# Kernel tuning notes

Hardware: AMD Instinct MI355X
Metric: run time of the kernel (lower is better)

The kernel has to match this reference:

```python
import jax, jax.numpy as jnp
import numpy as np

N, D, H, O, E = 50000, 512, 512, 256, 150000
NEG_SLOPE = 0.2
EPS = 1e-16


def gat_conv(x, edge_index, W_src, W_dst, a_src, a_dst, bias):
    """Single-head PyG GATConv, add_self_loops=False.
    x: [N, Din]; edge_index: [2, E] (row 0 = src, row 1 = dst).
    W_src/W_dst: [Din, C]; a_src/a_dst: [C]; bias: [C].
    """
    src, dst = edge_index[0], edge_index[1]
    h_src = x @ W_src                      # [N, C]
    h_dst = x @ W_dst                      # [N, C]
    alpha_src = h_src @ a_src              # [N]
    alpha_dst = h_dst @ a_dst              # [N]
    e = jax.nn.leaky_relu(alpha_src[src] + alpha_dst[dst], NEG_SLOPE)  # [E]
    # per-destination segment softmax (numerically stable)
    m = jax.ops.segment_max(e, dst, num_segments=N)       # [N]
    ex = jnp.exp(e - m[dst])                               # [E]
    s = jax.ops.segment_sum(ex, dst, num_segments=N)       # [N]
    alpha = ex / (s[dst] + EPS)                            # [E]
    # scatter-add weighted source messages to destinations
    out = jax.ops.segment_sum(alpha[:, None] * h_src[src], dst, num_segments=N)  # [N, C]
    return out + bias


def setup_inputs() -> dict:
    key = jax.random.key(0)
    ks = jax.random.split(key, 20)
    g = lambda i, shape, sc: (jax.random.normal(ks[i], shape, dtype=jnp.float32) * sc)
    inp = {
        "x": jax.random.normal(ks[0], (N, D), dtype=jnp.float32),
        "edge_index": jax.random.randint(ks[1], (2, E), 0, N, dtype=jnp.int32),
        "edge_index_2_hop": jax.random.randint(ks[2], (2, E), 0, N, dtype=jnp.int32),
        # conv1 (D -> H)
        "W1_src": g(3, (D, H), 0.05), "W1_dst": g(4, (D, H), 0.05),
        "a1_src": g(5, (H,), 0.05), "a1_dst": g(6, (H,), 0.05),
        "b1": jnp.zeros((H,), jnp.float32),
        # lin1 (H -> H)
        "Wl1": g(7, (H, H), 0.05), "bl1": jnp.zeros((H,), jnp.float32),
        # conv2 (H -> O)
        "W2_src": g(8, (H, O), 0.05), "W2_dst": g(9, (H, O), 0.05),
        "a2_src": g(10, (O,), 0.05), "a2_dst": g(11, (O,), 0.05),
        "b2": jnp.zeros((O,), jnp.float32),
        # lin2 (O -> O)
        "Wl2": g(12, (O, O), 0.05), "bl2": jnp.zeros((O,), jnp.float32),
    }
    return inp


def reference(x, edge_index, edge_index_2_hop,
              W1_src, W1_dst, a1_src, a1_dst, b1, Wl1, bl1,
              W2_src, W2_dst, a2_src, a2_dst, b2, Wl2, bl2):
    h = (gat_conv(x, edge_index, W1_src, W1_dst, a1_src, a1_dst, b1)
         + gat_conv(x, edge_index_2_hop, W1_src, W1_dst, a1_src, a1_dst, b1))
    h = jax.nn.relu(h @ Wl1 + bl1)
    h = (gat_conv(h, edge_index, W2_src, W2_dst, a2_src, a2_dst, b2)
         + gat_conv(h, edge_index_2_hop, W2_src, W2_dst, a2_src, a2_dst, b2))
    return h @ Wl2 + bl2
```

## Files before the change

### kernel.cpp

```cpp
#include <hip/hip_runtime.h>

typedef unsigned short u16;
typedef __attribute__((ext_vector_type(8))) unsigned short v8u16;
typedef __attribute__((ext_vector_type(4))) unsigned short v4u16;
typedef __attribute__((ext_vector_type(8))) __bf16 v8bf;
typedef __attribute__((ext_vector_type(4))) float v4f;

#define NN 50000
#define EE 150000
#define SCAN_CHUNK 512
#define NB_PER_SET 98

__device__ inline float b2f(u16 u) {
    union { unsigned int i; float f; } x; x.i = ((unsigned int)u) << 16; return x.f;
}
__device__ inline u16 f2b(float f) {
    union { float f; unsigned int i; } x; x.f = f;
    unsigned int r = x.i + 0x7FFFu + ((x.i >> 16) & 1u);
    return (u16)(r >> 16);
}
__device__ inline float wred(float v) {
    v += __shfl_down(v, 32, 64);
    v += __shfl_down(v, 16, 64);
    v += __shfl_down(v, 8, 64);
    v += __shfl_down(v, 4, 64);
    v += __shfl_down(v, 2, 64);
    v += __shfl_down(v, 1, 64);
    return v;
}
__device__ inline int wred_i(int v) {
    v += __shfl_down(v, 32, 64);
    v += __shfl_down(v, 16, 64);
    v += __shfl_down(v, 8, 64);
    v += __shfl_down(v, 4, 64);
    v += __shfl_down(v, 2, 64);
    v += __shfl_down(v, 1, 64);
    return v;
}

__device__ __forceinline__ void gll16(const u16* g, u16* l) {
    __builtin_amdgcn_global_load_lds(
        (const __attribute__((address_space(1))) void*)g,
        (__attribute__((address_space(3))) void*)l, 16, 0, 0);
}


__global__ void transpose4t(const float* __restrict__ W0, u16* __restrict__ T0,
                            const float* __restrict__ W1, u16* __restrict__ T1,
                            const float* __restrict__ W2, u16* __restrict__ T2,
                            const float* __restrict__ W3, u16* __restrict__ T3) {
    int b = blockIdx.x;
    const float* W; u16* T; int N, K, t;
    if (b < 256)      { W = W0; T = T0; K = 512; N = 512; t = b; }
    else if (b < 512) { W = W1; T = T1; K = 512; N = 512; t = b - 256; }
    else if (b < 640) { W = W2; T = T2; K = 512; N = 256; t = b - 512; }
    else              { W = W3; T = T3; K = 256; N = 256; t = b - 640; }
    const int tilesN = N >> 5;
    const int kb = (t / tilesN) << 5;
    const int nb = (t % tilesN) << 5;
    __shared__ u16 tile[32][33];
    const int c = threadIdx.x & 31;
    const int r0 = threadIdx.x >> 5;
#pragma unroll
    for (int rr = 0; rr < 4; ++rr) {
        int r = r0 + rr * 8;
        tile[r][c] = f2b(W[(size_t)(kb + r) * N + nb + c]);
    }
    __syncthreads();
#pragma unroll
    for (int rr = 0; rr < 4; ++rr) {
        int r = r0 + rr * 8;
        T[(size_t)(nb + r) * K + kb + c] = tile[c][r];
    }
}

__global__ void wv4(const float* __restrict__ Wa, const float* __restrict__ Wb,
                    const float* __restrict__ Wc, const float* __restrict__ Wd,
                    const float* __restrict__ aa, const float* __restrict__ ab,
                    const float* __restrict__ ac, const float* __restrict__ ad,
                    float* __restrict__ vbuf) {
    int rw = (blockIdx.x * blockDim.x + threadIdx.x) >> 6;
    int lane = threadIdx.x & 63;
    if (rw >= 2048) return;
    int seg = rw >> 9, r = rw & 511;
    const float* W; const float* a; int C;
    if (seg == 0)      { W = Wa; a = aa; C = 512; }
    else if (seg == 1) { W = Wb; a = ab; C = 512; }
    else if (seg == 2) { W = Wc; a = ac; C = 256; }
    else               { W = Wd; a = ad; C = 256; }
    float s = 0.f;
    int c0 = lane * 8;
    if (c0 < C) {
        const float* wp = W + (size_t)r * C + c0;
        v4f w0 = *(const v4f*)wp;
        v4f w1 = *(const v4f*)(wp + 4);
        v4f a0 = *(const v4f*)(a + c0);
        v4f a1 = *(const v4f*)(a + c0 + 4);
#pragma unroll
        for (int j = 0; j < 4; ++j) s += w0[j] * a0[j] + w1[j] * a1[j];
    }
    s = wred(s);
    if (lane == 0) vbuf[rw] = s;
}

__global__ void alpha_pair_f32x(const float* __restrict__ X, const float* __restrict__ vs,
                                const float* __restrict__ vd, float* __restrict__ as_,
                                float* __restrict__ ad_, u16* __restrict__ Xb, int Nn) {
    int w = (blockIdx.x * blockDim.x + threadIdx.x) >> 6;
    int lane = threadIdx.x & 63;
    if (w >= Nn) return;
    const float* xp = X + (size_t)w * 512 + lane * 8;
    v4f x0 = *(const v4f*)xp;
    v4f x1 = *(const v4f*)(xp + 4);
    const float* vsp = vs + lane * 8;
    const float* vdp = vd + lane * 8;
    float s1 = 0.f, s2 = 0.f;
    v8u16 o;
#pragma unroll
    for (int j = 0; j < 4; ++j) {
        s1 += x0[j] * vsp[j] + x1[j] * vsp[j + 4];
        s2 += x0[j] * vdp[j] + x1[j] * vdp[j + 4];
        o[j] = f2b(x0[j]); o[j + 4] = f2b(x1[j]);
    }
    *(v8u16*)(Xb + (size_t)w * 512 + lane * 8) = o;
    s1 = wred(s1);
    s2 = wred(s2);
    if (lane == 0) { as_[w] = s1; ad_[w] = s2; }
}


__global__ void deg2_kernel(const int* __restrict__ ei1, const int* __restrict__ ei2,
                            int* __restrict__ deg) {
    int idx = blockIdx.x * blockDim.x + threadIdx.x;
    if (idx >= 2 * EE) return;
    int set = idx >= EE;
    int e = idx - set * EE;
    const int* ei = set ? ei2 : ei1;
    atomicAdd(&deg[set * NN + ei[EE + e]], 1);
}

__global__ void scan_partial(const int* __restrict__ deg, int* __restrict__ bsum) {
    int b = blockIdx.x;
    int set = b / NB_PER_SET, lb = b - set * NB_PER_SET;
    int tid = threadIdx.x;
    int i0 = lb * SCAN_CHUNK + tid * 2;
    int s = 0;
    if (i0 < NN)     s += deg[set * NN + i0];
    if (i0 + 1 < NN) s += deg[set * NN + i0 + 1];
    s = wred_i(s);
    __shared__ int lsum[4];
    if ((tid & 63) == 0) lsum[tid >> 6] = s;
    __syncthreads();
    if (tid == 0) bsum[b] = lsum[0] + lsum[1] + lsum[2] + lsum[3];
}

__global__ void scan_tops(int* __restrict__ bsum) {
    __shared__ int ls[256];
    int tid = threadIdx.x;
    int set = tid >> 7, lb = tid & 127;
    int v = (lb < NB_PER_SET) ? bsum[set * NB_PER_SET + lb] : 0;
    ls[tid] = v;
    __syncthreads();
    for (int off = 1; off < 128; off <<= 1) {
        int t = (lb >= off) ? ls[tid - off] : 0;
        __syncthreads();
        ls[tid] += t;
        __syncthreads();
    }
    if (lb < NB_PER_SET) bsum[set * NB_PER_SET + lb] = ls[tid] - v;
}

__global__ void scan_final(const int* __restrict__ deg, const int* __restrict__ bsum,
                           int* __restrict__ rp) {
    int b = blockIdx.x;
    int set = b / NB_PER_SET, lb = b - set * NB_PER_SET;
    int tid = threadIdx.x;
    int i0 = lb * SCAN_CHUNK + tid * 2;
    int d0 = (i0 < NN)     ? deg[set * NN + i0]     : 0;
    int d1 = (i0 + 1 < NN) ? deg[set * NN + i0 + 1] : 0;
    int pair = d0 + d1;
    __shared__ int ps[256];
    ps[tid] = pair;
    __syncthreads();
    for (int off = 1; off < 256; off <<= 1) {
        int t = (tid >= off) ? ps[tid - off] : 0;
        __syncthreads();
        ps[tid] += t;
        __syncthreads();
    }
    int base = bsum[b] + ps[tid] - pair;
    if (i0 < NN)     rp[set * (NN + 1) + i0] = base;
    if (i0 + 1 < NN) rp[set * (NN + 1) + i0 + 1] = base + d0;
    if (b == 0 && tid == 0) { rp[NN] = EE; rp[(NN + 1) + NN] = EE; }
}

__global__ void fill2_kernel(const int* __restrict__ ei1, const int* __restrict__ ei2,
                             const int* __restrict__ rp, int* __restrict__ deg,
                             int* __restrict__ srcp) {
    int idx = blockIdx.x * blockDim.x + threadIdx.x;
    if (idx >= 2 * EE) return;
    int set = idx >= EE;
    int e = idx - set * EE;
    const int* ei = set ? ei2 : ei1;
    int d = ei[EE + e];
    int old = atomicSub(&deg[set * NN + d], 1);
    int pos = rp[set * (NN + 1) + d] + old - 1;
    srcp[set * EE + pos] = ei[e];
}

template <int CV>
__global__ void gat_pull(const int* __restrict__ rp, const int* __restrict__ srcp,
                         const float* __restrict__ asrc, const float* __restrict__ adst,
                         const u16* __restrict__ H, const float* __restrict__ bias,
                         u16* __restrict__ G, int Nn) {
    const int C = CV * 64;
    int d = (blockIdx.x * blockDim.x + threadIdx.x) >> 6;
    int lane = threadIdx.x & 63;
    if (d >= Nn) return;
    const float ad = adst[d];
    float out[CV];
#pragma unroll
    for (int j = 0; j < CV; ++j) out[j] = 0.f;
#pragma unroll
    for (int set = 0; set < 2; ++set) {
        const int* rpS = rp + set * (NN + 1);
        const int* srcS = srcp + set * EE;
        int beg = rpS[d], end = rpS[d + 1];
        float acc[CV];
#pragma unroll
        for (int j = 0; j < CV; ++j) acc[j] = 0.f;
        float ssum = 0.f;
        int n = end - beg;
        if (n > 0) {
            if constexpr (CV == 8) {
                int s0 = srcS[beg];
                float a0 = asrc[s0];
                v8u16 h0 = *(const v8u16*)(H + (size_t)s0 * C + lane * 8);
                float a1 = 0.f; v8u16 h1{};
                if (n > 1) {
                    int s1 = srcS[beg + 1];
                    a1 = asrc[s1];
                    h1 = *(const v8u16*)(H + (size_t)s1 * C + lane * 8);
                }
                for (int i = beg + 2; i < end; ++i) {
                    int s2 = srcS[i];
                    float a2 = asrc[s2];
                    v8u16 h2 = *(const v8u16*)(H + (size_t)s2 * C + lane * 8);
                    float t = a0 + ad; t = t > 0.f ? t : 0.2f * t;
                    float w = __expf(fminf(t, 60.f));
                    ssum += w;
#pragma unroll
                    for (int j = 0; j < 8; ++j) acc[j] += w * b2f(h0[j]);
                    a0 = a1; h0 = h1; a1 = a2; h1 = h2;
                }
                if (n > 1) {
                    float t = a0 + ad; t = t > 0.f ? t : 0.2f * t;
                    float w = __expf(fminf(t, 60.f));
                    ssum += w;
#pragma unroll
                    for (int j = 0; j < 8; ++j) acc[j] += w * b2f(h0[j]);
                    a0 = a1; h0 = h1;
                }
                float t = a0 + ad; t = t > 0.f ? t : 0.2f * t;
                float w = __expf(fminf(t, 60.f));
                ssum += w;
#pragma unroll
                for (int j = 0; j < 8; ++j) acc[j] += w * b2f(h0[j]);
            } else {
                int s0 = srcS[beg];
                float a0 = asrc[s0];
                v4u16 h0 = *(const v4u16*)(H + (size_t)s0 * C + lane * 4);
                float a1 = 0.f; v4u16 h1{};
                if (n > 1) {
                    int s1 = srcS[beg + 1];
                    a1 = asrc[s1];
                    h1 = *(const v4u16*)(H + (size_t)s1 * C + lane * 4);
                }
                for (int i = beg + 2; i < end; ++i) {
                    int s2 = srcS[i];
                    float a2 = asrc[s2];
                    v4u16 h2 = *(const v4u16*)(H + (size_t)s2 * C + lane * 4);
                    float t = a0 + ad; t = t > 0.f ? t : 0.2f * t;
                    float w = __expf(fminf(t, 60.f));
                    ssum += w;
#pragma unroll
                    for (int j = 0; j < 4; ++j) acc[j] += w * b2f(h0[j]);
                    a0 = a1; h0 = h1; a1 = a2; h1 = h2;
                }
                if (n > 1) {
                    float t = a0 + ad; t = t > 0.f ? t : 0.2f * t;
                    float w = __expf(fminf(t, 60.f));
                    ssum += w;
#pragma unroll
                    for (int j = 0; j < 4; ++j) acc[j] += w * b2f(h0[j]);
                    a0 = a1; h0 = h1;
                }
                float t = a0 + ad; t = t > 0.f ? t : 0.2f * t;
                float w = __expf(fminf(t, 60.f));
                ssum += w;
#pragma unroll
                for (int j = 0; j < 4; ++j) acc[j] += w * b2f(h0[j]);
            }
        }
        float inv = 1.f / (ssum + 1e-16f);
#pragma unroll
        for (int j = 0; j < CV; ++j) out[j] += acc[j] * inv;
    }
    const float* bp = bias + lane * CV;
    u16* gp = G + (size_t)d * C + lane * CV;
    if constexpr (CV == 8) {
        v8u16 o;
#pragma unroll
        for (int j = 0; j < 8; ++j) o[j] = f2b(out[j] + 2.f * bp[j]);
        *(v8u16*)gp = o;
    } else {
        v4u16 o;
#pragma unroll
        for (int j = 0; j < 4; ++j) o[j] = f2b(out[j] + 2.f * bp[j]);
        *(v4u16*)gp = o;
    }
}

__global__ __launch_bounds__(256, 3) void gemm_bf16(
    const u16* __restrict__ A, const u16* __restrict__ Bt, void* __restrict__ Cv,
    int M, int N, int K, const float* __restrict__ bias, int relu, int outf32,
    const float* __restrict__ avs, const float* __restrict__ avd,
    float* __restrict__ aout_s, float* __restrict__ aout_d) {
    __shared__ u16 As[128 * 32];
    __shared__ u16 Bs[128 * 32];
    const int tid = threadIdx.x;
    const int lane = tid & 63;
    const int wid = tid >> 6;
    const int wm = wid >> 1;
    const int wn = wid & 1;
    const int quad = lane >> 4;
    const int l16 = lane & 15;
    const int tileM = blockIdx.y * 128;
    const int tileN = blockIdx.x * 128;

    const int srow = tid >> 2;
    const int scol = (tid & 3) * 8;
    int ra0 = tileM + srow;       if (ra0 >= M) ra0 = M - 1;
    int ra1 = tileM + 64 + srow;  if (ra1 >= M) ra1 = M - 1;
    const u16* gA0 = A + (size_t)ra0 * K + scol;
    const u16* gA1 = A + (size_t)ra1 * K + scol;
    const u16* gB0 = Bt + (size_t)(tileN + srow) * K + scol;
    const u16* gB1 = Bt + (size_t)(tileN + 64 + srow) * K + scol;
    u16* lA0 = As + wid * 512;
    u16* lA1 = As + 2048 + wid * 512;
    u16* lB0 = Bs + wid * 512;
    u16* lB1 = Bs + 2048 + wid * 512;

    v4f acc[4][4];
#pragma unroll
    for (int i = 0; i < 4; ++i)
#pragma unroll
        for (int j = 0; j < 4; ++j) acc[i][j] = v4f{0.f, 0.f, 0.f, 0.f};

    for (int k0 = 0; k0 < K; k0 += 32) {
        gll16(gA0 + k0, lA0);
        gll16(gA1 + k0, lA1);
        gll16(gB0 + k0, lB0);
        gll16(gB1 + k0, lB1);
        __syncthreads();
        v8bf af[4], bfr[4];
#pragma unroll
        for (int i = 0; i < 4; ++i)
            af[i] = __builtin_bit_cast(v8bf, *(const v8u16*)&As[(wm * 64 + i * 16 + l16) * 32 + quad * 8]);
#pragma unroll
        for (int i = 0; i < 4; ++i)
            bfr[i] = __builtin_bit_cast(v8bf, *(const v8u16*)&Bs[(wn * 64 + i * 16 + l16) * 32 + quad * 8]);
#pragma unroll
        for (int mi = 0; mi < 4; ++mi)
#pragma unroll
            for (int ni = 0; ni < 4; ++ni)
                acc[mi][ni] = __builtin_amdgcn_mfma_f32_16x16x32_bf16(af[mi], bfr[ni], acc[mi][ni], 0, 0, 0);
        __syncthreads();
    }

    float rs[4][4], rd[4][4];
#pragma unroll
    for (int mi = 0; mi < 4; ++mi)
#pragma unroll
        for (int rr = 0; rr < 4; ++rr) { rs[mi][rr] = 0.f; rd[mi][rr] = 0.f; }

#pragma unroll
    for (int mi = 0; mi < 4; ++mi)
#pragma unroll
        for (int ni = 0; ni < 4; ++ni) {
            int col = tileN + wn * 64 + ni * 16 + l16;
            float bb = bias ? bias[col] : 0.f;
            float ws_ = avs ? avs[col] : 0.f;
            float wd_ = avd ? avd[col] : 0.f;
            int row0 = tileM + wm * 64 + mi * 16 + quad * 4;
#pragma unroll
            for (int rr = 0; rr < 4; ++rr) {
                int row = row0 + rr;
                if (row < M) {
                    float v = acc[mi][ni][rr] + bb;
                    if (relu) v = fmaxf(v, 0.f);
                    if (outf32) ((float*)Cv)[(size_t)row * N + col] = v;
                    else        ((u16*)Cv)[(size_t)row * N + col] = f2b(v);
                    rs[mi][rr] += v * ws_;
                    rd[mi][rr] += v * wd_;
                }
            }
        }

    if (avs) {
#pragma unroll
        for (int mi = 0; mi < 4; ++mi)
#pragma unroll
            for (int rr = 0; rr < 4; ++rr) {
                int row = tileM + wm * 64 + mi * 16 + quad * 4 + rr;
                float a = rs[mi][rr], b = rd[mi][rr];
                a += __shfl_down(a, 8, 64); a += __shfl_down(a, 4, 64);
                a += __shfl_down(a, 2, 64); a += __shfl_down(a, 1, 64);
                b += __shfl_down(b, 8, 64); b += __shfl_down(b, 4, 64);
                b += __shfl_down(b, 2, 64); b += __shfl_down(b, 1, 64);
                if (l16 == 0 && row < M) {
                    atomicAdd(&aout_s[row], a);
                    atomicAdd(&aout_d[row], b);
                }
            }
    }
}


extern "C" void kernel_launch(void* const* d_in, const int* in_sizes, int n_in,
                              void* d_out, int out_size, void* d_ws, size_t ws_size,
                              hipStream_t stream) {
    const float* x  = (const float*)d_in[0];
    const int* ei1  = (const int*)d_in[1];
    const int* ei2  = (const int*)d_in[2];
    const float* W1s = (const float*)d_in[3];
    const float* W1d = (const float*)d_in[4];
    const float* a1s = (const float*)d_in[5];
    const float* a1d = (const float*)d_in[6];
    const float* b1  = (const float*)d_in[7];
    const float* Wl1 = (const float*)d_in[8];
    const float* bl1 = (const float*)d_in[9];
    const float* W2s = (const float*)d_in[10];
    const float* W2d = (const float*)d_in[11];
    const float* a2s = (const float*)d_in[12];
    const float* a2d = (const float*)d_in[13];
    const float* b2  = (const float*)d_in[14];
    const float* Wl2 = (const float*)d_in[15];
    const float* bl2 = (const float*)d_in[16];
    float* out = (float*)d_out;

    char* ws = (char*)d_ws;
    size_t off = 0;
    auto alloc = [&](size_t b) { void* p = ws + off; off = (off + b + 255) & ~(size_t)255; return p; };
    u16* bufA   = (u16*)alloc((size_t)NN * 512 * 2);
    u16* bufB   = (u16*)alloc((size_t)NN * 512 * 2);
    int* rp     = (int*)alloc((size_t)2 * (NN + 1) * 4);
    int* srcp   = (int*)alloc((size_t)2 * EE * 4);
    int* zblk   = (int*)alloc((size_t)4 * NN * 4);
    int* deg    = zblk;
    float* asrc2 = (float*)(zblk + 2 * NN);
    float* adst2 = (float*)(zblk + 3 * NN);
    int* bsum   = (int*)alloc((size_t)2 * NB_PER_SET * 4);
    float* asrc = (float*)alloc((size_t)NN * 4);
    float* adst = (float*)alloc((size_t)NN * 4);
    float* vbuf = (float*)alloc(2048 * 4);
    u16* Wt1s   = (u16*)alloc((size_t)512 * 512 * 2);
    u16* Wtl1   = (u16*)alloc((size_t)512 * 512 * 2);
    u16* Wt2s   = (u16*)alloc((size_t)512 * 256 * 2);
    u16* Wtl2   = (u16*)alloc((size_t)256 * 256 * 2);
    u16* g2buf  = bufB + (size_t)NN * 256;

    hipMemsetAsync(zblk, 0, (size_t)4 * NN * 4, stream);
    deg2_kernel<<<(2 * EE + 255) / 256, 256, 0, stream>>>(ei1, ei2, deg);
    scan_partial<<<2 * NB_PER_SET, 256, 0, stream>>>(deg, bsum);
    scan_tops<<<1, 256, 0, stream>>>(bsum);
    scan_final<<<2 * NB_PER_SET, 256, 0, stream>>>(deg, bsum, rp);
    fill2_kernel<<<(2 * EE + 255) / 256, 256, 0, stream>>>(ei1, ei2, rp, deg, srcp);

    transpose4t<<<704, 256, 0, stream>>>(W1s, Wt1s, Wl1, Wtl1, W2s, Wt2s, Wl2, Wtl2);
    wv4<<<512, 256, 0, stream>>>(W1s, W1d, W2s, W2d, a1s, a1d, a2s, a2d, vbuf);

    alpha_pair_f32x<<<(NN + 3) / 4, 256, 0, stream>>>(x, vbuf, vbuf + 512, asrc, adst, bufB, NN);
    gemm_bf16<<<dim3(4, 391), 256, 0, stream>>>(bufB, Wt1s, bufA, NN, 512, 512, nullptr, 0, 0,
                                                nullptr, nullptr, nullptr, nullptr);
    gat_pull<8><<<(NN + 3) / 4, 256, 0, stream>>>(rp, srcp, asrc, adst, bufA, b1, bufB, NN);
    gemm_bf16<<<dim3(4, 391), 256, 0, stream>>>(bufB, Wtl1, bufA, NN, 512, 512, bl1, 1, 0,
                                                vbuf + 1024, vbuf + 1536, asrc2, adst2);

    gemm_bf16<<<dim3(2, 391), 256, 0, stream>>>(bufA, Wt2s, bufB, NN, 256, 512, nullptr, 0, 0,
                                                nullptr, nullptr, nullptr, nullptr);
    gat_pull<4><<<(NN + 3) / 4, 256, 0, stream>>>(rp, srcp, asrc2, adst2, bufB, b2, g2buf, NN);
    gemm_bf16<<<dim3(2, 391), 256, 0, stream>>>(g2buf, Wtl2, out, NN, 256, 256, bl2, 0, 1,
                                                nullptr, nullptr, nullptr, nullptr);

    (void)in_sizes; (void)n_in; (void)out_size; (void)ws_size;
}
```

Baseline: 514.6 us.

## Rewrite bf16 GEMM with 256x256 tiles, 4-stage LDS pipeline and swizzle

Replaces the 128x128 single-buffered GEMM with a 512-thread, 256x256-tile kernel. It uses a 4-deep ring of LDS buffers loaded asynchronously with explicit vmcnt waits, an XOR swizzle on LDS columns to reduce bank conflicts, and raised wave priority around the MFMA block. The aim is to overlap global loads with MFMA work and raise data reuse per tile. In exchange it uses much more LDS and more registers, and gives fewer blocks for the N=256 GEMMs, which risks lower occupancy and load imbalance.

```diff
diff --git a/kernel.cpp b/kernel.cpp
--- a/kernel.cpp
+++ b/kernel.cpp
@@ -321,78 +321,104 @@
     }
 }
 
-__global__ __launch_bounds__(256, 3) void gemm_bf16(
+__global__ __launch_bounds__(512, 2) void gemm_dp(
     const u16* __restrict__ A, const u16* __restrict__ Bt, void* __restrict__ Cv,
     int M, int N, int K, const float* __restrict__ bias, int relu, int outf32,
     const float* __restrict__ avs, const float* __restrict__ avd,
     float* __restrict__ aout_s, float* __restrict__ aout_d) {
-    __shared__ u16 As[128 * 32];
-    __shared__ u16 Bs[128 * 32];
+    __shared__ u16 As[4 * 8192];
+    __shared__ u16 Bs[4 * 8192];
     const int tid = threadIdx.x;
     const int lane = tid & 63;
     const int wid = tid >> 6;
-    const int wm = wid >> 1;
-    const int wn = wid & 1;
+    const int wm = wid >> 2;
+    const int wn = wid & 3;
     const int quad = lane >> 4;
     const int l16 = lane & 15;
-    const int tileM = blockIdx.y * 128;
-    const int tileN = blockIdx.x * 128;
+    const int tileM = blockIdx.y * 256;
+    const int tileN = blockIdx.x * 256;
 
     const int srow = tid >> 2;
-    const int scol = (tid & 3) * 8;
-    int ra0 = tileM + srow;       if (ra0 >= M) ra0 = M - 1;
-    int ra1 = tileM + 64 + srow;  if (ra1 >= M) ra1 = M - 1;
+    const int scol = 8 * ((tid & 3) ^ ((tid >> 2) & 3));
+    int ra0 = tileM + srow;        if (ra0 >= M) ra0 = M - 1;
+    int ra1 = tileM + 128 + srow;  if (ra1 >= M) ra1 = M - 1;
     const u16* gA0 = A + (size_t)ra0 * K + scol;
     const u16* gA1 = A + (size_t)ra1 * K + scol;
     const u16* gB0 = Bt + (size_t)(tileN + srow) * K + scol;
-    const u16* gB1 = Bt + (size_t)(tileN + 64 + srow) * K + scol;
+    const u16* gB1 = Bt + (size_t)(tileN + 128 + srow) * K + scol;
     u16* lA0 = As + wid * 512;
-    u16* lA1 = As + 2048 + wid * 512;
+    u16* lA1 = As + 4096 + wid * 512;
     u16* lB0 = Bs + wid * 512;
-    u16* lB1 = Bs + 2048 + wid * 512;
-
-    v4f acc[4][4];
-#pragma unroll
-    for (int i = 0; i < 4; ++i)
+    u16* lB1 = Bs + 4096 + wid * 512;
+
+    v4f acc[8][4];
+#pragma unroll
+    for (int i = 0; i < 8; ++i)
 #pragma unroll
         for (int j = 0; j < 4; ++j) acc[i][j] = v4f{0.f, 0.f, 0.f, 0.f};
 
-    for (int k0 = 0; k0 < K; k0 += 32) {
-        gll16(gA0 + k0, lA0);
-        gll16(gA1 + k0, lA1);
-        gll16(gB0 + k0, lB0);
-        gll16(gB1 + k0, lB1);
-        __syncthreads();
-        v8bf af[4], bfr[4];
-#pragma unroll
-        for (int i = 0; i < 4; ++i)
-            af[i] = __builtin_bit_cast(v8bf, *(const v8u16*)&As[(wm * 64 + i * 16 + l16) * 32 + quad * 8]);
-#pragma unroll
-        for (int i = 0; i < 4; ++i)
-            bfr[i] = __builtin_bit_cast(v8bf, *(const v8u16*)&Bs[(wn * 64 + i * 16 + l16) * 32 + quad * 8]);
-#pragma unroll
-        for (int mi = 0; mi < 4; ++mi)
-#pragma unroll
-            for (int ni = 0; ni < 4; ++ni)
-                acc[mi][ni] = __builtin_amdgcn_mfma_f32_16x16x32_bf16(af[mi], bfr[ni], acc[mi][ni], 0, 0, 0);
-        __syncthreads();
-    }
-
-    float rs[4][4], rd[4][4];
-#pragma unroll
-    for (int mi = 0; mi < 4; ++mi)
-#pragma unroll
-        for (int rr = 0; rr < 4; ++rr) { rs[mi][rr] = 0.f; rd[mi][rr] = 0.f; }
-
-#pragma unroll
-    for (int mi = 0; mi < 4; ++mi)
+    const int T = K >> 5;
+
+#define STAGE(bb, kk)                                   \
+    do {                                                \
+        int o = (bb) * 8192;                            \
+        gll16(gA0 + (kk), lA0 + o);                     \
+        gll16(gA1 + (kk), lA1 + o);                     \
+        gll16(gB0 + (kk), lB0 + o);                     \
+        gll16(gB1 + (kk), lB1 + o);                     \
+    } while (0)
+
+    STAGE(0, 0);
+    STAGE(1, 32);
+    STAGE(2, 64);
+
+    for (int t = 0; t < T; ++t) {
+        if (t + 3 < T) STAGE((t + 3) & 3, (t + 3) << 5);
+        __builtin_amdgcn_sched_barrier(0);
+        if (t + 3 < T)      asm volatile("s_waitcnt vmcnt(12)" ::: "memory");
+        else if (t + 2 < T) asm volatile("s_waitcnt vmcnt(8)" ::: "memory");
+        else if (t + 1 < T) asm volatile("s_waitcnt vmcnt(4)" ::: "memory");
+        else                asm volatile("s_waitcnt vmcnt(0)" ::: "memory");
+        __builtin_amdgcn_s_barrier();
+        __builtin_amdgcn_sched_barrier(0);
+        {
+            const u16* a_ = As + (t & 3) * 8192;
+            const u16* b_ = Bs + (t & 3) * 8192;
+            const int pb = (quad ^ (l16 & 3)) * 8;
+            v8bf af[8], bf[4];
+#pragma unroll
+            for (int mi = 0; mi < 8; ++mi) {
+                int row = wm * 128 + mi * 16 + l16;
+                af[mi] = __builtin_bit_cast(v8bf, *(const v8u16*)&a_[row * 32 + pb]);
+            }
+#pragma unroll
+            for (int ni = 0; ni < 4; ++ni) {
+                int row = wn * 64 + ni * 16 + l16;
+                bf[ni] = __builtin_bit_cast(v8bf, *(const v8u16*)&b_[row * 32 + pb]);
+            }
+            __builtin_amdgcn_s_setprio(1);
+#pragma unroll
+            for (int mi = 0; mi < 8; ++mi)
+#pragma unroll
+                for (int ni = 0; ni < 4; ++ni)
+                    acc[mi][ni] = __builtin_amdgcn_mfma_f32_16x16x32_bf16(af[mi], bf[ni], acc[mi][ni], 0, 0, 0);
+            __builtin_amdgcn_s_setprio(0);
+        }
+        __builtin_amdgcn_sched_barrier(0);
+        __builtin_amdgcn_s_barrier();
+    }
+#undef STAGE
+
+#pragma unroll 1
+    for (int mi = 0; mi < 8; ++mi) {
+        float rs[4] = {0.f, 0.f, 0.f, 0.f}, rd[4] = {0.f, 0.f, 0.f, 0.f};
 #pragma unroll
         for (int ni = 0; ni < 4; ++ni) {
             int col = tileN + wn * 64 + ni * 16 + l16;
             float bb = bias ? bias[col] : 0.f;
             float ws_ = avs ? avs[col] : 0.f;
             float wd_ = avd ? avd[col] : 0.f;
-            int row0 = tileM + wm * 64 + mi * 16 + quad * 4;
+            int row0 = tileM + wm * 128 + mi * 16 + quad * 4;
 #pragma unroll
             for (int rr = 0; rr < 4; ++rr) {
                 int row = row0 + rr;
@@ -401,19 +427,16 @@
                     if (relu) v = fmaxf(v, 0.f);
                     if (outf32) ((float*)Cv)[(size_t)row * N + col] = v;
                     else        ((u16*)Cv)[(size_t)row * N + col] = f2b(v);
-                    rs[mi][rr] += v * ws_;
-                    rd[mi][rr] += v * wd_;
+                    rs[rr] += v * ws_;
+                    rd[rr] += v * wd_;
                 }
             }
         }
-
-    if (avs) {
-#pragma unroll
-        for (int mi = 0; mi < 4; ++mi)
+        if (avs) {
 #pragma unroll
             for (int rr = 0; rr < 4; ++rr) {
-                int row = tileM + wm * 64 + mi * 16 + quad * 4 + rr;
-                float a = rs[mi][rr], b = rd[mi][rr];
+                int row = tileM + wm * 128 + mi * 16 + quad * 4 + rr;
+                float a = rs[rr], b = rd[rr];
                 a += __shfl_down(a, 8, 64); a += __shfl_down(a, 4, 64);
                 a += __shfl_down(a, 2, 64); a += __shfl_down(a, 1, 64);
                 b += __shfl_down(b, 8, 64); b += __shfl_down(b, 4, 64);
@@ -423,6 +446,7 @@
                     atomicAdd(&aout_d[row], b);
                 }
             }
+        }
     }
 }
 
@@ -480,18 +504,20 @@
     transpose4t<<<704, 256, 0, stream>>>(W1s, Wt1s, Wl1, Wtl1, W2s, Wt2s, Wl2, Wtl2);
     wv4<<<512, 256, 0, stream>>>(W1s, W1d, W2s, W2d, a1s, a1d, a2s, a2d, vbuf);
 
+    const int MT = (NN + 255) / 256;
+
     alpha_pair_f32x<<<(NN + 3) / 4, 256, 0, stream>>>(x, vbuf, vbuf + 512, asrc, adst, bufB, NN);
-    gemm_bf16<<<dim3(4, 391), 256, 0, stream>>>(bufB, Wt1s, bufA, NN, 512, 512, nullptr, 0, 0,
-                                                nullptr, nullptr, nullptr, nullptr);
+    gemm_dp<<<dim3(2, MT), 512, 0, stream>>>(bufB, Wt1s, bufA, NN, 512, 512, nullptr, 0, 0,
+                                             nullptr, nullptr, nullptr, nullptr);
     gat_pull<8><<<(NN + 3) / 4, 256, 0, stream>>>(rp, srcp, asrc, adst, bufA, b1, bufB, NN);
-    gemm_bf16<<<dim3(4, 391), 256, 0, stream>>>(bufB, Wtl1, bufA, NN, 512, 512, bl1, 1, 0,
-                                                vbuf + 1024, vbuf + 1536, asrc2, adst2);
-
-    gemm_bf16<<<dim3(2, 391), 256, 0, stream>>>(bufA, Wt2s, bufB, NN, 256, 512, nullptr, 0, 0,
-                                                nullptr, nullptr, nullptr, nullptr);
+    gemm_dp<<<dim3(2, MT), 512, 0, stream>>>(bufB, Wtl1, bufA, NN, 512, 512, bl1, 1, 0,
+                                             vbuf + 1024, vbuf + 1536, asrc2, adst2);
+
+    gemm_dp<<<dim3(1, MT), 512, 0, stream>>>(bufA, Wt2s, bufB, NN, 256, 512, nullptr, 0, 0,
+                                             nullptr, nullptr, nullptr, nullptr);
     gat_pull<4><<<(NN + 3) / 4, 256, 0, stream>>>(rp, srcp, asrc2, adst2, bufB, b2, g2buf, NN);
-    gemm_bf16<<<dim3(2, 391), 256, 0, stream>>>(g2buf, Wtl2, out, NN, 256, 256, bl2, 0, 1,
-                                                nullptr, nullptr, nullptr, nullptr);
+    gemm_dp<<<dim3(1, MT), 512, 0, stream>>>(g2buf, Wtl2, out, NN, 256, 256, bl2, 0, 1,
+                                             nullptr, nullptr, nullptr, nullptr);
 
     (void)in_sizes; (void)n_in; (void)out_size; (void)ws_size;
 }
```

New measurement: 835.3 us. 1.62x slower.
